# Kernel tuning notes

Measured on AMD Instinct MI355X. Metric: run time of the kernel, lower is better.

The kernel has to match this reference:

```python
import math
import jax
import jax.numpy as jnp
import numpy as np

B, Q, K, D = 8, 2048, 2048, 256
TOP_K = 64
NEG = -1000000.0


def setup_inputs() -> dict:
    key = jax.random.key(0)
    kq, kk, kv, kl = jax.random.split(key, 4)
    return {
        "queries": jax.random.normal(kq, (B, Q, D), dtype=jnp.float32),
        "keys": jax.random.normal(kk, (B, K, D), dtype=jnp.float32),
        "values": jax.random.normal(kv, (B, K, D), dtype=jnp.float32),
        "valid_lens": jax.random.randint(kl, (B,), 0, 2048, dtype=jnp.int32),
    }


def reference(queries, keys, values, valid_lens):
    d = queries.shape[-1]
    # [B, Q, K] scaled dot-product scores
    scores = jnp.einsum("bqd,bkd->bqk", queries, keys) / math.sqrt(d)
    # valid-length mask over key axis (same valid_len for every query row in a batch)
    key_mask = jnp.arange(scores.shape[-1]) < valid_lens[:, None, None]  # [B,1,K]
    scores = jnp.where(key_mask, scores, NEG)
    # per-row top-k threshold: keep scores >= k-th largest
    topk = min(TOP_K, scores.shape[-1])
    kth = jax.lax.top_k(scores, topk)[0][:, :, -1:]  # [B,Q,1]
    scores = jnp.where(scores < kth, NEG, scores)
    attn = jax.nn.softmax(scores, axis=-1)
    return jnp.einsum("bqk,bkv->bqv", attn, values)
```

## Files before the change

### kernel.cpp

```cpp
#include <hip/hip_runtime.h>


#define QN 2048
#define KN 2048
#define DN 256
#define NEGV (-1000000.0f)
#define PC 128
#define CAP 200u
#define CAPP 201
#define TRIG 72u
#define MARGIN 3e-4f

typedef __attribute__((ext_vector_type(8))) short short8;
typedef __attribute__((ext_vector_type(4))) float f32x4;

union U4S8 { uint4 u; short8 s; };

__device__ __forceinline__ unsigned sortkey(unsigned b) {
  return b ^ (unsigned)((((int)b) >> 31) | 0x80000000u);
}
__device__ __forceinline__ float keytofloat(unsigned k) {
  unsigned b = (k & 0x80000000u) ? (k ^ 0x80000000u) : ~k;
  return __uint_as_float(b);
}
__device__ __forceinline__ unsigned long long sortkey64(double d) {
  long long b = __double_as_longlong(d);
  return (unsigned long long)(b ^ ((b >> 63) | 0x8000000000000000LL));
}
__device__ __forceinline__ unsigned pack_hi(unsigned a, unsigned b) {
  return (b & 0xFFFF0000u) | (a >> 16);
}

__device__ __forceinline__ void split8(const float4& x0, const float4& x1,
                                       short8& hi8, short8& lo8) {
  float f[8] = {x0.x, x0.y, x0.z, x0.w, x1.x, x1.y, x1.z, x1.w};
  unsigned hw[4], lw[4];
#pragma unroll
  for (int i = 0; i < 4; ++i) {
    unsigned a = __float_as_uint(f[2 * i]);
    unsigned b = __float_as_uint(f[2 * i + 1]);
    hw[i] = pack_hi(a, b);
    float ra = f[2 * i]     - __uint_as_float(a & 0xFFFF0000u);
    float rb = f[2 * i + 1] - __uint_as_float(b & 0xFFFF0000u);
    lw[i] = pack_hi(__float_as_uint(ra), __float_as_uint(rb));
  }
  U4S8 h, l;
  h.u = make_uint4(hw[0], hw[1], hw[2], hw[3]);
  l.u = make_uint4(lw[0], lw[1], lw[2], lw[3]);
  hi8 = h.s;
  lo8 = l.s;
}

__global__ __launch_bounds__(256, 2) void sparse_attn(const float* __restrict__ Q,
                                                      const float* __restrict__ K,
                                                      const float* __restrict__ V,
                                                      const int* __restrict__ vlens,
                                                      float* __restrict__ out) {
  __shared__ float S[32][PC];
  __shared__ uint2 pool[32][CAPP];
  __shared__ unsigned cnt[32];
  __shared__ unsigned Lb[32];
  __shared__ unsigned nqs[32];
  __shared__ float rden[32];

  const unsigned tid = threadIdx.x;
  const unsigned w = tid >> 6, lane = tid & 63u;
  const unsigned lm = lane & 15u, lg = lane >> 4;
  const unsigned bid = blockIdx.x;
  const unsigned b = bid >> 6, qt = bid & 63u;
  const int vlen = vlens[b];
  const unsigned long long below = (1ull << lane) - 1ull;

  if (vlen == 0) {
    float* PS = (float*)&pool[0][0];
    unsigned g = tid >> 3, ds = tid & 7u;
    float4 s[8];
#pragma unroll
    for (int j = 0; j < 8; ++j) s[j] = make_float4(0.f, 0.f, 0.f, 0.f);
    const float* Vb = V + (size_t)b * KN * DN;
    for (int i = 0; i < 64; ++i) {
      const float* vr = Vb + (size_t)(g * 64u + i) * DN + ds * 32u;
#pragma unroll
      for (int j = 0; j < 8; ++j) {
        float4 vv = *(const float4*)(vr + j * 4);
        s[j].x += vv.x; s[j].y += vv.y; s[j].z += vv.z; s[j].w += vv.w;
      }
    }
#pragma unroll
    for (int j = 0; j < 8; ++j)
      *(float4*)&PS[g * 256u + ds * 32u + j * 4] = s[j];
    __syncthreads();
    float mval = 0.f;
    for (int g2 = 0; g2 < 32; ++g2) mval += PS[g2 * 256 + tid];
    PS[8192 + tid] = mval * (1.0f / 2048.0f);
    __syncthreads();
    unsigned row = tid >> 3;
    float* op = out + ((size_t)(b * QN + qt * 32u + row)) * DN + ds * 32u;
#pragma unroll
    for (int j = 0; j < 8; ++j)
      *(float4*)(op + j * 4) = *(const float4*)&PS[8192 + ds * 32u + j * 4];
    return;
  }

  if (tid < 32) { cnt[tid] = 0u; Lb[tid] = 0u; }
  __syncthreads();

  short8 qh[2][8], ql[2][8];
#pragma unroll
  for (int rt = 0; rt < 2; ++rt) {
    const float* qrow = Q + ((size_t)(b * QN + qt * 32u + rt * 16u + lm)) * DN;
#pragma unroll
    for (int c = 0; c < 8; ++c) {
      const float* src = qrow + c * 32u + lg * 8u;
      float4 x0 = *(const float4*)(src);
      float4 x1 = *(const float4*)(src + 4);
      split8(x0, x1, qh[rt][c], ql[rt][c]);
    }
  }

  const float* Kb = K + (size_t)b * KN * DN;
  unsigned nparts = ((unsigned)vlen + (PC - 1)) / PC;
  if (nparts > 16u) nparts = 16u;

  for (unsigned p = 0; p < nparts; ++p) {
    f32x4 acc[2][2];
#pragma unroll
    for (int rt = 0; rt < 2; ++rt)
#pragma unroll
      for (int j = 0; j < 2; ++j) acc[rt][j] = (f32x4){0.f, 0.f, 0.f, 0.f};

    unsigned colbase = p * PC + w * 32u;
#pragma unroll
    for (int c = 0; c < 8; ++c) {
#pragma unroll
      for (int j = 0; j < 2; ++j) {
        const float* src = Kb + (size_t)(colbase + j * 16u + lm) * DN + c * 32u + lg * 8u;
        float4 x0 = *(const float4*)(src);
        float4 x1 = *(const float4*)(src + 4);
        short8 kh, kl;
        split8(x0, x1, kh, kl);
        acc[0][j] = __builtin_amdgcn_mfma_f32_16x16x32_bf16(qh[0][c], kh, acc[0][j], 0, 0, 0);
        acc[1][j] = __builtin_amdgcn_mfma_f32_16x16x32_bf16(qh[1][c], kh, acc[1][j], 0, 0, 0);
        acc[0][j] = __builtin_amdgcn_mfma_f32_16x16x32_bf16(ql[0][c], kh, acc[0][j], 0, 0, 0);
        acc[1][j] = __builtin_amdgcn_mfma_f32_16x16x32_bf16(ql[1][c], kh, acc[1][j], 0, 0, 0);
        acc[0][j] = __builtin_amdgcn_mfma_f32_16x16x32_bf16(qh[0][c], kl, acc[0][j], 0, 0, 0);
        acc[1][j] = __builtin_amdgcn_mfma_f32_16x16x32_bf16(qh[1][c], kl, acc[1][j], 0, 0, 0);
      }
    }

#pragma unroll
    for (int rt = 0; rt < 2; ++rt)
#pragma unroll
      for (int j = 0; j < 2; ++j)
#pragma unroll
        for (int r = 0; r < 4; ++r) {
          unsigned row = rt * 16u + lg * 4u + r;
          unsigned col = w * 32u + j * 16u + lm;
          float v = acc[rt][j][r] * 0.0625f;
          if (p * PC + col >= (unsigned)vlen) v = NEGV;
          S[row][col] = v;
        }
    __syncthreads();

    for (int rr = 0; rr < 8; ++rr) {
      unsigned row = w * 8u + rr;
      unsigned L = Lb[row];
#pragma unroll
      for (int i = 0; i < 2; ++i) {
        unsigned cidx = lane + 64u * i;
        float v = S[row][cidx];
        unsigned kk = sortkey(__float_as_uint(v));
        bool qual = (v != NEGV) && (kk >= L);
        unsigned long long mask = __ballot(qual);
        if (mask) {
          int ldr = __ffsll((unsigned long long)mask) - 1;
          unsigned base = 0;
          if ((int)lane == ldr) base = atomicAdd(&cnt[row], (unsigned)__popcll(mask));
          base = __shfl(base, ldr);
          unsigned pos = base + (unsigned)__popcll(mask & below);
          if (qual && pos < CAP)
            pool[row][pos] = make_uint2(__float_as_uint(v), p * PC + cidx);
        }
      }
      unsigned n = cnt[row]; if (n > CAP) n = CAP;
      if (n > TRIG) {
        bool val[4]; uint2 e[4]; unsigned key[4]; float f[4];
#pragma unroll
        for (int t = 0; t < 4; ++t) {
          unsigned idx = lane + 64u * t;
          val[t] = idx < n;
          e[t] = val[t] ? pool[row][idx] : make_uint2(0u, 0u);
          key[t] = val[t] ? sortkey(e[t].x) : 0u;
          f[t] = val[t] ? __uint_as_float(e[t].x) : -3.4e38f;
        }
        unsigned lo = 0u, hi = 0xFFFFFFF0u;
        for (int it = 0; it < 34 && lo < hi; ++it) {
          unsigned mid = lo + ((hi - lo + 1u) >> 1);
          int c = 0;
#pragma unroll
          for (int t = 0; t < 4; ++t) c += (int)__popcll(__ballot(key[t] >= mid));
          if (c == 64) { lo = mid; break; }
          if (c > 64) lo = mid; else hi = mid - 1u;
        }
        float thrf = keytofloat(lo) - MARGIN;
        unsigned nn = 0;
#pragma unroll
        for (int t = 0; t < 4; ++t) {
          bool q = val[t] && (f[t] >= thrf);
          unsigned long long mk = __ballot(q);
          if (q) pool[row][nn + (unsigned)__popcll(mk & below)] = e[t];
          nn += (unsigned)__popcll(mk);
        }
        if (lane == 0) { cnt[row] = nn; Lb[row] = sortkey(__float_as_uint(thrf)); }
      }
    }
    __syncthreads();
  }

  for (int rr = 0; rr < 8; ++rr) {
    unsigned row = w * 8u + rr;
    unsigned n = cnt[row]; if (n > CAP) n = CAP;
    bool val[4]; uint2 e[4]; unsigned key[4]; float f[4];
#pragma unroll
    for (int t = 0; t < 4; ++t) {
      unsigned idx = lane + 64u * t;
      val[t] = idx < n;
      e[t] = val[t] ? pool[row][idx] : make_uint2(0u, 0u);
      key[t] = val[t] ? sortkey(e[t].x) : 0u;
      f[t] = val[t] ? __uint_as_float(e[t].x) : -3.4e38f;
    }
    bool sel[4];
    if (n > 64u) {
      unsigned lo = 0u, hi = 0xFFFFFFF0u;
      for (int it = 0; it < 34 && lo < hi; ++it) {
        unsigned mid = lo + ((hi - lo + 1u) >> 1);
        int c = 0;
#pragma unroll
        for (int t = 0; t < 4; ++t) c += (int)__popcll(__ballot(key[t] >= mid));
        if (c == 64) { lo = mid; break; }
        if (c > 64) lo = mid; else hi = mid - 1u;
      }
      float m64f = keytofloat(lo);
      float hi_thr = m64f + MARGIN, lo_thr = m64f - MARGIN;
      bool def_[4], band[4];
      int ndef = 0;
#pragma unroll
      for (int t = 0; t < 4; ++t) {
        def_[t] = val[t] && (f[t] >= hi_thr);
        band[t] = val[t] && !def_[t] && (f[t] >= lo_thr);
        ndef += (int)__popcll(__ballot(def_[t]));
      }
      const float* qrow = Q + ((size_t)(b * QN + qt * 32u + row)) * DN;
      float4 qv = *(const float4*)(qrow + lane * 4u);
      unsigned long long K64[4] = {0ull, 0ull, 0ull, 0ull};
#pragma unroll
      for (int t = 0; t < 4; ++t) {
        unsigned long long mk = __ballot(band[t]);
        while (mk) {
          int src = __ffsll(mk) - 1;
          mk &= mk - 1ull;
          unsigned col = (unsigned)__shfl((int)e[t].y, src);
          const float4 kv = *(const float4*)(Kb + (size_t)col * DN + lane * 4u);
          double s = fma((double)qv.x, (double)kv.x,
                     fma((double)qv.y, (double)kv.y,
                     fma((double)qv.z, (double)kv.z,
                         (double)qv.w * (double)kv.w)));
#pragma unroll
          for (int off = 32; off > 0; off >>= 1) s += __shfl_xor(s, off);
          if ((int)lane == src) K64[t] = sortkey64(s * 0.0625);
        }
      }
      bool rem[4];
#pragma unroll
      for (int t = 0; t < 4; ++t) { sel[t] = def_[t]; rem[t] = band[t]; }
      int sc = ndef;
      while (sc < 64) {
        unsigned long long mv = 0ull;
#pragma unroll
        for (int t = 0; t < 4; ++t)
          if (rem[t] && K64[t] > mv) mv = K64[t];
#pragma unroll
        for (int off = 32; off > 0; off >>= 1) {
          unsigned long long o = __shfl_xor(mv, off);
          if (o > mv) mv = o;
        }
        bool picked = false;
#pragma unroll
        for (int t = 0; t < 4; ++t) {
          if (!picked) {
            unsigned long long mk = __ballot(rem[t] && K64[t] == mv);
            if (mk) {
              if ((int)lane == __ffsll(mk) - 1) { rem[t] = false; sel[t] = true; }
              picked = true;
            }
          }
        }
        ++sc;
        if (!picked) break;
      }
    } else {
#pragma unroll
      for (int t = 0; t < 4; ++t) sel[t] = val[t];
    }

    float mx = -3.4e38f;
#pragma unroll
    for (int t = 0; t < 4; ++t) if (val[t]) mx = fmaxf(mx, f[t]);
#pragma unroll
    for (int off = 32; off > 0; off >>= 1) mx = fmaxf(mx, __shfl_xor(mx, off));
    float wv[4];
    float zs = 0.f;
#pragma unroll
    for (int t = 0; t < 4; ++t) {
      wv[t] = sel[t] ? expf(f[t] - mx) : 0.f;
      zs += wv[t];
    }
#pragma unroll
    for (int off = 32; off > 0; off >>= 1) zs += __shfl_xor(zs, off);

    unsigned nn = 0;
#pragma unroll
    for (int t = 0; t < 4; ++t) {
      unsigned long long mk = __ballot(sel[t]);
      if (sel[t])
        pool[row][nn + (unsigned)__popcll(mk & below)] =
            make_uint2(__float_as_uint(wv[t]), e[t].y);
      nn += (unsigned)__popcll(mk);
    }
    if (lane == 0) { nqs[row] = nn; rden[row] = 1.0f / zs; }
  }
  __syncthreads();

  {
    unsigned grow = tid >> 3, gds = tid & 7u;
    unsigned gnq = nqs[grow];
    float rd = rden[grow];
    float4 a[8];
#pragma unroll
    for (int j = 0; j < 8; ++j) a[j] = make_float4(0.f, 0.f, 0.f, 0.f);
    const float* Vb = V + (size_t)b * KN * DN;
    for (unsigned ei = 0; ei < gnq; ++ei) {
      uint2 pe = pool[grow][ei];
      float wvv = __uint_as_float(pe.x);
      const float* vr = Vb + (size_t)pe.y * DN + gds * 32u;
#pragma unroll
      for (int j = 0; j < 8; ++j) {
        float4 vv = *(const float4*)(vr + j * 4);
        a[j].x = fmaf(wvv, vv.x, a[j].x);
        a[j].y = fmaf(wvv, vv.y, a[j].y);
        a[j].z = fmaf(wvv, vv.z, a[j].z);
        a[j].w = fmaf(wvv, vv.w, a[j].w);
      }
    }
    float* op = out + ((size_t)(b * QN + qt * 32u + grow)) * DN + gds * 32u;
#pragma unroll
    for (int j = 0; j < 8; ++j) {
      float4 r = make_float4(a[j].x * rd, a[j].y * rd, a[j].z * rd, a[j].w * rd);
      *(float4*)(op + j * 4) = r;
    }
  }
}

extern "C" void kernel_launch(void* const* d_in, const int* in_sizes, int n_in,
                              void* d_out, int out_size, void* d_ws, size_t ws_size,
                              hipStream_t stream) {
  (void)in_sizes; (void)n_in; (void)out_size; (void)d_ws; (void)ws_size;
  const float* Q = (const float*)d_in[0];
  const float* K = (const float*)d_in[1];
  const float* V = (const float*)d_in[2];
  const int* vl = (const int*)d_in[3];
  float* out = (float*)d_out;
  sparse_attn<<<dim3(512), dim3(256), 0, stream>>>(Q, K, V, vl, out);
}
```

Baseline: 536.8 us.

## Split fused sparse attention into score GEMM, vsum, and per-row top-k/PV kernels

When enough workspace is available, the single fused kernel is replaced by three kernels. A tiled split-bf16 MFMA GEMM writes the full score matrix to global memory, a small kernel precomputes value column sums for the vlen==0 case, and a one-wave-per-row kernel selects the top-k from registers, refines borderline candidates in fp64, and does the sparse PV. The aim is more parallelism than the 512-block fused kernel, at the cost of a 128 MB score round trip through HBM. The old fused kernel is kept as a fallback when the workspace is too small.

```diff
diff --git a/kernel.cpp b/kernel.cpp
--- a/kernel.cpp
+++ b/kernel.cpp
@@ -5,11 +5,9 @@
 #define KN 2048
 #define DN 256
 #define NEGV (-1000000.0f)
-#define PC 128
-#define CAP 200u
-#define CAPP 201
-#define TRIG 72u
-#define MARGIN 3e-4f
+#define MARGIN 1e-3f
+#define WS_NEED 134225920ull
+#define BANDCAP 48
 
 typedef __attribute__((ext_vector_type(8))) short short8;
 typedef __attribute__((ext_vector_type(4))) float f32x4;
@@ -51,12 +49,274 @@
   lo8 = l.s;
 }
 
-__global__ __launch_bounds__(256, 2) void sparse_attn(const float* __restrict__ Q,
-                                                      const float* __restrict__ K,
-                                                      const float* __restrict__ V,
-                                                      const int* __restrict__ vlens,
-                                                      float* __restrict__ out) {
-  __shared__ float S[32][PC];
+__device__ __forceinline__ void split4(const float4& x, uint2& hu, uint2& lu) {
+  unsigned a0 = __float_as_uint(x.x), a1 = __float_as_uint(x.y);
+  unsigned a2 = __float_as_uint(x.z), a3 = __float_as_uint(x.w);
+  hu.x = pack_hi(a0, a1);
+  hu.y = pack_hi(a2, a3);
+  float r0 = x.x - __uint_as_float(a0 & 0xFFFF0000u);
+  float r1 = x.y - __uint_as_float(a1 & 0xFFFF0000u);
+  float r2 = x.z - __uint_as_float(a2 & 0xFFFF0000u);
+  float r3 = x.w - __uint_as_float(a3 & 0xFFFF0000u);
+  lu.x = pack_hi(__float_as_uint(r0), __float_as_uint(r1));
+  lu.y = pack_hi(__float_as_uint(r2), __float_as_uint(r3));
+}
+
+__global__ __launch_bounds__(256) void score_gemm(const float* __restrict__ Q,
+                                                  const float* __restrict__ K,
+                                                  const int* __restrict__ vlens,
+                                                  float* __restrict__ S) {
+  __shared__ unsigned short KT[128][64];
+
+  const unsigned tid = threadIdx.x;
+  const unsigned w = tid >> 6, lane = tid & 63u;
+  const unsigned lm = lane & 15u, lg = lane >> 4;
+  const unsigned bid = blockIdx.x;
+  const unsigned b = bid >> 9;
+  const unsigned r9 = bid & 511u;
+  const unsigned ct = r9 >> 5, qt = r9 & 31u;
+  const int vlen = vlens[b];
+  const unsigned colbase = ct * 128u;
+  if ((int)colbase >= vlen) return;
+
+  short8 qh[8], ql[8];
+  const float* qrow = Q + ((size_t)(b * QN + qt * 64u + w * 16u + lm)) * DN;
+#pragma unroll
+  for (int c = 0; c < 8; ++c) {
+    float4 x0 = *(const float4*)(qrow + c * 32 + lg * 8);
+    float4 x1 = *(const float4*)(qrow + c * 32 + lg * 8 + 4);
+    split8(x0, x1, qh[c], ql[c]);
+  }
+
+  f32x4 acc[8];
+#pragma unroll
+  for (int j = 0; j < 8; ++j) acc[j] = (f32x4){0.f, 0.f, 0.f, 0.f};
+
+  for (unsigned c = 0; c < 8; ++c) {
+    __syncthreads();
+#pragma unroll
+    for (int i = 0; i < 4; ++i) {
+      unsigned col = (tid >> 3) + i * 32u;
+      unsigned gi = (tid >> 1) & 3u;
+      unsigned h2 = tid & 1u;
+      const float4 v = *(const float4*)(K + ((size_t)(b * KN + colbase + col)) * DN +
+                                        c * 32u + gi * 8u + h2 * 4u);
+      uint2 hu, lu;
+      split4(v, hu, lu);
+      unsigned slot = gi ^ (col & 3u);
+      *(uint2*)&KT[col][slot * 8u + h2 * 4u] = hu;
+      *(uint2*)&KT[col][32u + slot * 8u + h2 * 4u] = lu;
+    }
+    __syncthreads();
+#pragma unroll
+    for (int j = 0; j < 8; ++j) {
+      unsigned col = j * 16u + lm;
+      unsigned slot = lg ^ (col & 3u);
+      short8 kh = *(const short8*)&KT[col][slot * 8u];
+      short8 kl = *(const short8*)&KT[col][32u + slot * 8u];
+      acc[j] = __builtin_amdgcn_mfma_f32_16x16x32_bf16(qh[c], kh, acc[j], 0, 0, 0);
+      acc[j] = __builtin_amdgcn_mfma_f32_16x16x32_bf16(ql[c], kh, acc[j], 0, 0, 0);
+      acc[j] = __builtin_amdgcn_mfma_f32_16x16x32_bf16(qh[c], kl, acc[j], 0, 0, 0);
+    }
+  }
+
+  float* Sb = S + ((size_t)b * QN + qt * 64u + w * 16u) * (size_t)KN + colbase;
+#pragma unroll
+  for (int j = 0; j < 8; ++j)
+#pragma unroll
+    for (int r = 0; r < 4; ++r)
+      Sb[(size_t)(lg * 4u + r) * KN + j * 16u + lm] = acc[j][r] * 0.0625f;
+}
+
+__global__ __launch_bounds__(256) void vsum_kernel(const float* __restrict__ V,
+                                                   float* __restrict__ vsum) {
+  __shared__ float red[8][32];
+  unsigned b = blockIdx.x >> 3, chunk = blockIdx.x & 7u;
+  unsigned c = threadIdx.x & 31u, s = threadIdx.x >> 5;
+  unsigned col = chunk * 32u + c;
+  const float* base = V + ((size_t)b * KN + s * 256u) * DN + col;
+  float acc = 0.f;
+#pragma unroll 8
+  for (int r = 0; r < 256; ++r) acc += base[(size_t)r * DN];
+  red[s][c] = acc;
+  __syncthreads();
+  if (s == 0) {
+    float t = 0.f;
+#pragma unroll
+    for (int j = 0; j < 8; ++j) t += red[j][c];
+    vsum[b * DN + col] = t;
+  }
+}
+
+__global__ __launch_bounds__(256) void topk_pv(const float* __restrict__ Q,
+                                               const float* __restrict__ K,
+                                               const float* __restrict__ V,
+                                               const int* __restrict__ vlens,
+                                               const float* __restrict__ S,
+                                               const float* __restrict__ vsum,
+                                               float* __restrict__ out) {
+  __shared__ uint2 selbuf[4][64];
+  __shared__ unsigned long long bkey[4][BANDCAP];
+  __shared__ unsigned bcol[4][BANDCAP];
+  __shared__ unsigned char bpicked[4][BANDCAP];
+
+  const unsigned tid = threadIdx.x, w = tid >> 6, lane = tid & 63u;
+  const size_t row = (size_t)blockIdx.x * 4u + w;
+  const unsigned b = (unsigned)(row >> 11);
+  const int vlen = vlens[b];
+  float* orow = out + row * DN;
+  const unsigned long long below = (1ull << lane) - 1ull;
+
+  if (vlen == 0) {
+    const float4 sv = *(const float4*)(vsum + (size_t)b * DN + lane * 4u);
+    const float cc = 1.0f / 2048.0f;
+    *(float4*)(orow + lane * 4u) = make_float4(sv.x * cc, sv.y * cc, sv.z * cc, sv.w * cc);
+    return;
+  }
+
+  const float* Srow = S + row * (size_t)KN;
+  float v[32];
+#pragma unroll
+  for (int i = 0; i < 8; ++i) {
+    float4 x = *(const float4*)(Srow + i * 256u + lane * 4u);
+    int c0 = i * 256 + (int)lane * 4;
+    v[i * 4 + 0] = (c0 + 0 < vlen) ? x.x : -3.4e38f;
+    v[i * 4 + 1] = (c0 + 1 < vlen) ? x.y : -3.4e38f;
+    v[i * 4 + 2] = (c0 + 2 < vlen) ? x.z : -3.4e38f;
+    v[i * 4 + 3] = (c0 + 3 < vlen) ? x.w : -3.4e38f;
+  }
+
+  unsigned selm = 0u;
+  if (vlen <= 64) {
+#pragma unroll
+    for (int k = 0; k < 32; ++k)
+      if (v[k] > -1e30f) selm |= (1u << k);
+  } else {
+    unsigned key[32];
+#pragma unroll
+    for (int k = 0; k < 32; ++k) key[k] = sortkey(__float_as_uint(v[k]));
+    unsigned lo = 0u, hi = 0xFFFFFFF0u;
+    for (int it = 0; it < 34 && lo < hi; ++it) {
+      unsigned mid = lo + ((hi - lo + 1u) >> 1);
+      int c = 0;
+#pragma unroll
+      for (int k = 0; k < 32; ++k)
+        c += (int)__popcll(__ballot(key[k] >= mid));
+      if (c == 64) { lo = mid; break; }
+      if (c > 64) lo = mid; else hi = mid - 1u;
+    }
+    float m64f = keytofloat(lo);
+    float hi_thr = m64f + MARGIN;
+    float lo_thr = m64f - MARGIN;
+
+    unsigned defm = 0u, bandm = 0u;
+    int ndef = 0;
+#pragma unroll
+    for (int k = 0; k < 32; ++k) {
+      bool d = v[k] >= hi_thr;
+      bool bd = !d && (v[k] >= lo_thr);
+      if (d) defm |= (1u << k);
+      if (bd) bandm |= (1u << k);
+      ndef += (int)d;
+    }
+#pragma unroll
+    for (int off = 32; off > 0; off >>= 1) ndef += __shfl_xor(ndef, off);
+
+    const float4 qv = *(const float4*)(Q + ((size_t)b * QN + (unsigned)(row & 2047u)) * DN + lane * 4u);
+    const float* Kb = K + (size_t)b * KN * DN;
+    int nb = 0;
+#pragma unroll
+    for (int k = 0; k < 32; ++k) {
+      unsigned long long mk = __ballot((bandm >> k) & 1u);
+      while (mk && nb < BANDCAP) {
+        int src = __ffsll(mk) - 1;
+        mk &= mk - 1ull;
+        unsigned col = ((unsigned)(k >> 2)) * 256u + (unsigned)src * 4u + (unsigned)(k & 3);
+        const float4 kv = *(const float4*)(Kb + (size_t)col * DN + lane * 4u);
+        double s = fma((double)qv.x, (double)kv.x,
+                   fma((double)qv.y, (double)kv.y,
+                   fma((double)qv.z, (double)kv.z,
+                       (double)qv.w * (double)kv.w)));
+#pragma unroll
+        for (int off = 32; off > 0; off >>= 1) s += __shfl_xor(s, off);
+        if (lane == 0) {
+          bkey[w][nb] = sortkey64(s * 0.0625);
+          bcol[w][nb] = col;
+          bpicked[w][nb] = 0;
+        }
+        ++nb;
+      }
+    }
+
+    selm = defm;
+    int need = 64 - ndef;
+    for (int pi = 0; pi < need; ++pi) {
+      unsigned long long best = 0ull;
+      int bj = -1;
+      for (int j2 = 0; j2 < nb; ++j2)
+        if (!bpicked[w][j2] && bkey[w][j2] > best) { best = bkey[w][j2]; bj = j2; }
+      if (bj < 0) break;
+      if (lane == 0) bpicked[w][bj] = 1;
+      unsigned col = bcol[w][bj];
+      unsigned owner = (col >> 2) & 63u;
+      unsigned kreg = ((col >> 8) << 2) | (col & 3u);
+      if (lane == owner) selm |= (1u << kreg);
+    }
+  }
+
+  float mx = -3.4e38f;
+#pragma unroll
+  for (int k = 0; k < 32; ++k)
+    if ((selm >> k) & 1u) mx = fmaxf(mx, v[k]);
+#pragma unroll
+  for (int off = 32; off > 0; off >>= 1) mx = fmaxf(mx, __shfl_xor(mx, off));
+
+  float zs = 0.f;
+  unsigned base = 0;
+#pragma unroll
+  for (int k = 0; k < 32; ++k) {
+    bool s1 = (selm >> k) & 1u;
+    unsigned long long mk = __ballot(s1);
+    float wt = s1 ? __expf(v[k] - mx) : 0.f;
+    zs += wt;
+    if (s1) {
+      unsigned pos = base + (unsigned)__popcll(mk & below);
+      unsigned col = ((unsigned)(k >> 2)) * 256u + lane * 4u + (unsigned)(k & 3);
+      selbuf[w][pos] = make_uint2(__float_as_uint(wt), col);
+    }
+    base += (unsigned)__popcll(mk);
+  }
+#pragma unroll
+  for (int off = 32; off > 0; off >>= 1) zs += __shfl_xor(zs, off);
+  unsigned nsel = base;
+
+  float4 a = make_float4(0.f, 0.f, 0.f, 0.f);
+  const float* Vb = V + (size_t)b * KN * DN;
+  for (unsigned e = 0; e < nsel; ++e) {
+    uint2 pe = selbuf[w][e];
+    float wt = __uint_as_float(pe.x);
+    const float4 vv = *(const float4*)(Vb + (size_t)pe.y * DN + lane * 4u);
+    a.x = fmaf(wt, vv.x, a.x);
+    a.y = fmaf(wt, vv.y, a.y);
+    a.z = fmaf(wt, vv.z, a.z);
+    a.w = fmaf(wt, vv.w, a.w);
+  }
+  float rz = 1.0f / zs;
+  *(float4*)(orow + lane * 4u) = make_float4(a.x * rz, a.y * rz, a.z * rz, a.w * rz);
+}
+
+#define PC 128
+#define CAP 200u
+#define CAPP 201
+#define TRIG 72u
+#define FMARGIN 3e-4f
+
+__global__ __launch_bounds__(256, 2) void sparse_attn_fused(const float* __restrict__ Q,
+                                                            const float* __restrict__ K,
+                                                            const float* __restrict__ V,
+                                                            const int* __restrict__ vlens,
+                                                            float* __restrict__ out) {
+  __shared__ float Sm[32][PC];
   __shared__ uint2 pool[32][CAPP];
   __shared__ unsigned cnt[32];
   __shared__ unsigned Lb[32];
@@ -154,11 +414,11 @@
       for (int j = 0; j < 2; ++j)
 #pragma unroll
         for (int r = 0; r < 4; ++r) {
-          unsigned row = rt * 16u + lg * 4u + r;
+          unsigned rrow = rt * 16u + lg * 4u + r;
           unsigned col = w * 32u + j * 16u + lm;
-          float v = acc[rt][j][r] * 0.0625f;
-          if (p * PC + col >= (unsigned)vlen) v = NEGV;
-          S[row][col] = v;
+          float vv = acc[rt][j][r] * 0.0625f;
+          if (p * PC + col >= (unsigned)vlen) vv = NEGV;
+          Sm[rrow][col] = vv;
         }
     __syncthreads();
 
@@ -168,18 +428,18 @@
 #pragma unroll
       for (int i = 0; i < 2; ++i) {
         unsigned cidx = lane + 64u * i;
-        float v = S[row][cidx];
-        unsigned kk = sortkey(__float_as_uint(v));
-        bool qual = (v != NEGV) && (kk >= L);
+        float vv = Sm[row][cidx];
+        unsigned kk = sortkey(__float_as_uint(vv));
+        bool qual = (vv != NEGV) && (kk >= L);
         unsigned long long mask = __ballot(qual);
         if (mask) {
           int ldr = __ffsll((unsigned long long)mask) - 1;
-          unsigned base = 0;
-          if ((int)lane == ldr) base = atomicAdd(&cnt[row], (unsigned)__popcll(mask));
-          base = __shfl(base, ldr);
-          unsigned pos = base + (unsigned)__popcll(mask & below);
+          unsigned bse = 0;
+          if ((int)lane == ldr) bse = atomicAdd(&cnt[row], (unsigned)__popcll(mask));
+          bse = __shfl(bse, ldr);
+          unsigned pos = bse + (unsigned)__popcll(mask & below);
           if (qual && pos < CAP)
-            pool[row][pos] = make_uint2(__float_as_uint(v), p * PC + cidx);
+            pool[row][pos] = make_uint2(__float_as_uint(vv), p * PC + cidx);
         }
       }
       unsigned n = cnt[row]; if (n > CAP) n = CAP;
@@ -202,7 +462,7 @@
           if (c == 64) { lo = mid; break; }
           if (c > 64) lo = mid; else hi = mid - 1u;
         }
-        float thrf = keytofloat(lo) - MARGIN;
+        float thrf = keytofloat(lo) - FMARGIN;
         unsigned nn = 0;
 #pragma unroll
         for (int t = 0; t < 4; ++t) {
@@ -241,7 +501,7 @@
         if (c > 64) lo = mid; else hi = mid - 1u;
       }
       float m64f = keytofloat(lo);
-      float hi_thr = m64f + MARGIN, lo_thr = m64f - MARGIN;
+      float hi_thr = m64f + FMARGIN, lo_thr = m64f - FMARGIN;
       bool def_[4], band[4];
       int ndef = 0;
 #pragma unroll
@@ -303,31 +563,37 @@
       for (int t = 0; t < 4; ++t) sel[t] = val[t];
     }
 
-    float mx = -3.4e38f;
-#pragma unroll
-    for (int t = 0; t < 4; ++t) if (val[t]) mx = fmaxf(mx, f[t]);
-#pragma unroll
-    for (int off = 32; off > 0; off >>= 1) mx = fmaxf(mx, __shfl_xor(mx, off));
-    float wv[4];
-    float zs = 0.f;
-#pragma unroll
-    for (int t = 0; t < 4; ++t) {
-      wv[t] = sel[t] ? expf(f[t] - mx) : 0.f;
-      zs += wv[t];
-    }
-#pragma unroll
-    for (int off = 32; off > 0; off >>= 1) zs += __shfl_xor(zs, off);
+    float mv2 = -3.4e38f;
+#pragma unroll
+    for (int t = 0; t < 4; ++t) if (val[t]) mv2 = fmaxf(mv2, f[t]);
+#pragma unroll
+    for (int off = 32; off > 0; off >>= 1) mv2 = fmaxf(mv2, __shfl_xor(mv2, off));
+
+    bool q0 = sel[0], q1 = sel[1], q2 = sel[2], q3 = sel[3];
+    float w0 = q0 ? __expf(f[0] - mv2) : 0.f;
+    float w1 = q1 ? __expf(f[1] - mv2) : 0.f;
+    float w2 = q2 ? __expf(f[2] - mv2) : 0.f;
+    float w3 = q3 ? __expf(f[3] - mv2) : 0.f;
+    float ws2 = w0 + w1 + w2 + w3;
+#pragma unroll
+    for (int off = 32; off > 0; off >>= 1) ws2 += __shfl_xor(ws2, off);
 
     unsigned nn = 0;
-#pragma unroll
-    for (int t = 0; t < 4; ++t) {
-      unsigned long long mk = __ballot(sel[t]);
-      if (sel[t])
-        pool[row][nn + (unsigned)__popcll(mk & below)] =
-            make_uint2(__float_as_uint(wv[t]), e[t].y);
+    {
+      unsigned long long mk = __ballot(q0);
+      if (q0) pool[row][nn + (unsigned)__popcll(mk & below)] = make_uint2(__float_as_uint(w0), e[0].y);
       nn += (unsigned)__popcll(mk);
-    }
-    if (lane == 0) { nqs[row] = nn; rden[row] = 1.0f / zs; }
+      mk = __ballot(q1);
+      if (q1) pool[row][nn + (unsigned)__popcll(mk & below)] = make_uint2(__float_as_uint(w1), e[1].y);
+      nn += (unsigned)__popcll(mk);
+      mk = __ballot(q2);
+      if (q2) pool[row][nn + (unsigned)__popcll(mk & below)] = make_uint2(__float_as_uint(w2), e[2].y);
+      nn += (unsigned)__popcll(mk);
+      mk = __ballot(q3);
+      if (q3) pool[row][nn + (unsigned)__popcll(mk & below)] = make_uint2(__float_as_uint(w3), e[3].y);
+      nn += (unsigned)__popcll(mk);
+    }
+    if (lane == 0) { nqs[row] = nn; rden[row] = 1.0f / ws2; }
   }
   __syncthreads();
 
@@ -364,11 +630,20 @@
 extern "C" void kernel_launch(void* const* d_in, const int* in_sizes, int n_in,
                               void* d_out, int out_size, void* d_ws, size_t ws_size,
                               hipStream_t stream) {
-  (void)in_sizes; (void)n_in; (void)out_size; (void)d_ws; (void)ws_size;
+  (void)in_sizes; (void)n_in; (void)out_size;
   const float* Q = (const float*)d_in[0];
   const float* K = (const float*)d_in[1];
   const float* V = (const float*)d_in[2];
   const int* vl = (const int*)d_in[3];
   float* out = (float*)d_out;
-  sparse_attn<<<dim3(512), dim3(256), 0, stream>>>(Q, K, V, vl, out);
-}
+
+  if (ws_size >= WS_NEED) {
+    float* S = (float*)d_ws;
+    float* vsum = (float*)((char*)d_ws + 134217728ull);
+    score_gemm<<<dim3(4096), dim3(256), 0, stream>>>(Q, K, vl, S);
+    vsum_kernel<<<dim3(64), dim3(256), 0, stream>>>(V, vsum);
+    topk_pv<<<dim3(4096), dim3(256), 0, stream>>>(Q, K, V, vl, S, vsum, out);
+  } else {
+    sparse_attn_fused<<<dim3(512), dim3(256), 0, stream>>>(Q, K, V, vl, out);
+  }
+}
```

Result: slower. 650.4 us (+21.2%).
